# Performance work log

Hardware: AMD Instinct MI355X
Metric: run time of the kernel (lower is better)

## Reference

```python
import jax, jax.numpy as jnp
import numpy as np

B, C, N, M = 4096, 1024, 256, 64
EPS = 1e-8


def _linear_params(key, out_dim, in_dim):
    kw, kb = jax.random.split(key)
    lim = 1.0 / np.sqrt(in_dim)
    W = jax.random.uniform(kw, (out_dim, in_dim), jnp.float32, -lim, lim)
    b = jax.random.uniform(kb, (out_dim,), jnp.float32, -lim, lim)
    return W, b


def setup_inputs() -> dict:
    key = jax.random.key(0)
    ks = jax.random.split(key, 10)
    emb = jax.random.normal(ks[0], (B, C), jnp.float32)
    w_prev = jax.random.uniform(ks[1], (B, N), jnp.float32)
    w_prev = w_prev / jnp.sum(w_prev, axis=1, keepdims=True)  # valid weighting
    memory = jax.random.normal(ks[2], (B, N, M), jnp.float32) * 0.1
    Wk, bk = _linear_params(ks[3], M, C)
    Wbeta, bbeta = _linear_params(ks[4], 1, C)
    Wg, bg = _linear_params(ks[5], 1, C)
    Ws, bs = _linear_params(ks[6], 3, C)
    Wgamma, bgamma = _linear_params(ks[7], 1, C)
    We, be = _linear_params(ks[8], M, C)
    Wa, ba = _linear_params(ks[9], M, C)
    return {
        'embeddings': emb, 'w_prev': w_prev, 'memory': memory,
        'Wk': Wk, 'bk': bk, 'Wbeta': Wbeta, 'bbeta': bbeta,
        'Wg': Wg, 'bg': bg, 'Ws': Ws, 'bs': bs,
        'Wgamma': Wgamma, 'bgamma': bgamma,
        'We': We, 'be': be, 'Wa': Wa, 'ba': ba,
    }


def _forward(embeddings, w_prev, memory, Wk, bk, Wbeta, bbeta, Wg, bg,
             Ws, bs, Wgamma, bgamma, We, be, Wa, ba):
    k = embeddings @ Wk.T + bk                                  # [B, M]
    beta = jax.nn.softplus(embeddings @ Wbeta.T + bbeta)        # [B, 1]
    g = jax.nn.sigmoid(embeddings @ Wg.T + bg)                  # [B, 1]
    s = jax.nn.softmax(embeddings @ Ws.T + bs, axis=1)          # [B, 3]
    gamma = 1.0 + jax.nn.softplus(embeddings @ Wgamma.T + bgamma)  # [B, 1]
    e = jax.nn.sigmoid(embeddings @ We.T + be)                  # [B, M]
    a = embeddings @ Wa.T + ba                                  # [B, M]

    # content addressing: beta-scaled cosine similarity + softmax
    dot = jnp.einsum('bnm,bm->bn', memory, k)                   # [B, N]
    mem_norm = jnp.linalg.norm(memory, axis=-1)                 # [B, N]
    k_norm = jnp.linalg.norm(k, axis=-1, keepdims=True)         # [B, 1]
    cos = dot / (jnp.maximum(mem_norm, EPS) * jnp.maximum(k_norm, EPS))
    w_c = jax.nn.softmax(beta * cos, axis=1)                    # [B, N]

    # interpolation gate
    w_g = g * w_c + (1.0 - g) * w_prev                          # [B, N]

    # circular 3-tap shift: c[i] = s0*w[i-1] + s1*w[i] + s2*w[i+1]
    w_s = (s[:, 0:1] * jnp.roll(w_g, 1, axis=1)
           + s[:, 1:2] * w_g
           + s[:, 2:3] * jnp.roll(w_g, -1, axis=1))             # [B, N]

    # sharpen
    w_pow = jnp.power(w_s, gamma)                               # [B, N]
    w = w_pow / (jnp.sum(w_pow, axis=1, keepdims=True) + 1e-16)

    # erase / add write (outer products)
    erase = w[:, :, None] * e[:, None, :]                       # [B, N, M]
    add = w[:, :, None] * a[:, None, :]                         # [B, N, M]
    new_memory = memory * (1.0 - erase) + add
    return w, new_memory


def reference(embeddings, w_prev, memory, Wk, bk, Wbeta, bbeta, Wg, bg,
              Ws, bs, Wgamma, bgamma, We, be, Wa, ba):
    return _forward(embeddings, w_prev, memory, Wk, bk, Wbeta, bbeta,
                    Wg, bg, Ws, bs, Wgamma, bgamma, We, be, Wa, ba)
```

## Files before the change

### kernel.cpp

```cpp
#include <hip/hip_runtime.h>
#include <hip/hip_bf16.h>

#define B_DIM 4096
#define C_DIM 1024
#define N_DIM 256
#define M_DIM 64
#define GPAD  208
#define NG    198
#define EPSC  1e-8f
#define PDS   17

typedef __attribute__((ext_vector_type(8))) short bfrag_t;
typedef __attribute__((ext_vector_type(4))) float ffrag_t;

__device__ __forceinline__ short f2b(float f) {
    __hip_bfloat16 h = __float2bfloat16(f);
    return *reinterpret_cast<short*>(&h);
}
__device__ __forceinline__ float softplus_f(float x) {
    return fmaxf(x, 0.f) + log1pf(expf(-fabsf(x)));
}
__device__ __forceinline__ float sigmoid_f(float x) {
    return 1.f / (1.f + expf(-x));
}
__device__ __forceinline__ float warp_red_max(float v) {
#pragma unroll
    for (int off = 32; off; off >>= 1) v = fmaxf(v, __shfl_xor(v, off));
    return v;
}
__device__ __forceinline__ float warp_red_sum(float v) {
#pragma unroll
    for (int off = 32; off; off >>= 1) v += __shfl_xor(v, off);
    return v;
}

__global__ __launch_bounds__(256) void build_wcat(
    const float* __restrict__ Wk, const float* __restrict__ Wbeta,
    const float* __restrict__ Wg, const float* __restrict__ Ws,
    const float* __restrict__ Wgamma, const float* __restrict__ We,
    const float* __restrict__ Wa, short* __restrict__ wcat)
{
    int idx = blockIdx.x * 256 + threadIdx.x;
    if (idx >= GPAD * C_DIM) return;
    int n = idx >> 10, k = idx & (C_DIM - 1);
    float v;
    if (n < 64)        v = Wk[n * C_DIM + k];
    else if (n == 64)  v = Wbeta[k];
    else if (n == 65)  v = Wg[k];
    else if (n < 69)   v = Ws[(n - 66) * C_DIM + k];
    else if (n == 69)  v = Wgamma[k];
    else if (n < 134)  v = We[(n - 70) * C_DIM + k];
    else if (n < NG)   v = Wa[(n - 134) * C_DIM + k];
    else               v = 0.f;
    wcat[idx] = f2b(v);
}

__global__ __launch_bounds__(256) void cvt_emb(
    const float* __restrict__ emb, short* __restrict__ embh)
{
    int idx = (blockIdx.x * 256 + threadIdx.x) << 3;
    if (idx >= B_DIM * C_DIM) return;
    float4 a0 = *(const float4*)(emb + idx);
    float4 a1 = *(const float4*)(emb + idx + 4);
    bfrag_t f;
    f[0] = f2b(a0.x); f[1] = f2b(a0.y); f[2] = f2b(a0.z); f[3] = f2b(a0.w);
    f[4] = f2b(a1.x); f[5] = f2b(a1.y); f[6] = f2b(a1.z); f[7] = f2b(a1.w);
    *(bfrag_t*)(embh + idx) = f;
}

__global__ __launch_bounds__(256) void gates_gemm(
    const short* __restrict__ embh,
    const short* __restrict__ wcat,
    float* __restrict__ gates)
{
    const int wave = threadIdx.x >> 6;
    const int lane = threadIdx.x & 63;
    const int rg   = blockIdx.x >> 2;
    const int tt   = ((blockIdx.x & 3) << 2) + wave;
    if (tt >= 13) return;

    const int m  = lane & 15;
    const int ko = (lane >> 4) << 3;

    const short* arow = embh + (size_t)(rg * 16 + m) * C_DIM + ko;
    const short* brow = wcat + (size_t)(tt * 16 + m) * C_DIM + ko;

    ffrag_t acc = (ffrag_t)(0.f);
#pragma unroll 4
    for (int k = 0; k < C_DIM; k += 32) {
        bfrag_t af = *(const bfrag_t*)(arow + k);
        bfrag_t bf = *(const bfrag_t*)(brow + k);
        acc = __builtin_amdgcn_mfma_f32_16x16x32_bf16(af, bf, acc, 0, 0, 0);
    }

    const int crow = rg * 16 + ((lane >> 4) << 2);
    const int n = (tt << 4) + m;
#pragma unroll
    for (int rr = 0; rr < 4; ++rr)
        gates[(size_t)(crow + rr) * GPAD + n] = acc[rr];
}

__global__ __launch_bounds__(256, 4) void ntm_fused(
    const float* __restrict__ w_prev,
    const float* __restrict__ memory,
    const float* __restrict__ gates,
    const float* __restrict__ bk, const float* __restrict__ bbeta,
    const float* __restrict__ bg, const float* __restrict__ bs,
    const float* __restrict__ bgamma, const float* __restrict__ be,
    const float* __restrict__ ba,
    float* __restrict__ out_w,
    float* __restrict__ out_mem)
{
    const int b = blockIdx.x;
    const int t = threadIdx.x;
    const int r = t >> 4;
    const int c = t & 15;

    __shared__ __align__(16) float pdot[N_DIM * PDS];
    __shared__ __align__(16) float pnrm[N_DIM * PDS];
    __shared__ __align__(16) float pre[NG];
    __shared__ __align__(16) float kvf[M_DIM];
    __shared__ __align__(16) float ev[M_DIM];
    __shared__ __align__(16) float av[M_DIM];
    __shared__ float wgs[N_DIM];
    __shared__ float wsh[N_DIM];
    __shared__ float scal[8];
    __shared__ float redA[4], redB[4], redC[4];

    const float4* msrc = (const float4*)(memory + (size_t)b * (N_DIM * M_DIM));
    float4 v[16];
#pragma unroll
    for (int i = 0; i < 16; ++i) v[i] = msrc[t + (i << 8)];

    float wprev_t = w_prev[(size_t)b * N_DIM + t];
    if (t < NG) pre[t] = gates[(size_t)b * GPAD + t];
    __syncthreads();

    if (t < 64) {
        float kt = pre[t] + bk[t];
        kvf[t] = kt;
        ev[t]  = sigmoid_f(pre[70 + t] + be[t]);
        av[t]  = pre[134 + t] + ba[t];
        float sq = warp_red_sum(kt * kt);
        if (t == 0) scal[6] = sqrtf(sq);
    }
    if (t == 64) {
        scal[0] = softplus_f(pre[64] + bbeta[0]);
        scal[1] = sigmoid_f(pre[65] + bg[0]);
        float x0 = pre[66] + bs[0];
        float x1 = pre[67] + bs[1];
        float x2 = pre[68] + bs[2];
        float mxs = fmaxf(x0, fmaxf(x1, x2));
        float e0 = expf(x0 - mxs), e1 = expf(x1 - mxs), e2 = expf(x2 - mxs);
        float inv = 1.f / (e0 + e1 + e2);
        scal[3] = e0 * inv; scal[4] = e1 * inv; scal[5] = e2 * inv;
        scal[2] = 1.f + softplus_f(pre[69] + bgamma[0]);
    }
    __syncthreads();

    float4 kc = *(const float4*)&kvf[c << 2];
#pragma unroll
    for (int i = 0; i < 16; ++i) {
        float d, q;
        d = v[i].x * kc.x;          q = v[i].x * v[i].x;
        d = fmaf(v[i].y, kc.y, d);  q = fmaf(v[i].y, v[i].y, q);
        d = fmaf(v[i].z, kc.z, d);  q = fmaf(v[i].z, v[i].z, q);
        d = fmaf(v[i].w, kc.w, d);  q = fmaf(v[i].w, v[i].w, q);
        int n = r + (i << 4);
        pdot[n * PDS + c] = d;
        pnrm[n * PDS + c] = q;
    }
    __syncthreads();

    float dot = 0.f, nrm = 0.f;
#pragma unroll
    for (int j = 0; j < 16; ++j) {
        dot += pdot[t * PDS + j];
        nrm += pnrm[t * PDS + j];
    }

    float cosv = dot / (fmaxf(sqrtf(nrm), EPSC) * fmaxf(scal[6], EPSC));
    float x = scal[0] * cosv;

    float mx = warp_red_max(x);
    if ((t & 63) == 0) redA[t >> 6] = mx;
    __syncthreads();
    mx = fmaxf(fmaxf(redA[0], redA[1]), fmaxf(redA[2], redA[3]));
    float ex = expf(x - mx);
    float sm_ = warp_red_sum(ex);
    if ((t & 63) == 0) redB[t >> 6] = sm_;
    __syncthreads();
    float wc = ex / (redB[0] + redB[1] + redB[2] + redB[3]);

    float g = scal[1];
    float wg = g * wc + (1.f - g) * wprev_t;
    wgs[t] = wg;
    __syncthreads();

    float ws_ = scal[3] * wgs[(t + 255) & 255] + scal[4] * wg + scal[5] * wgs[(t + 1) & 255];

    float wp = powf(fmaxf(ws_, 0.f), scal[2]);
    float ts = warp_red_sum(wp);
    if ((t & 63) == 0) redC[t >> 6] = ts;
    __syncthreads();
    float w = wp / (redC[0] + redC[1] + redC[2] + redC[3] + 1e-16f);

    out_w[(size_t)b * N_DIM + t] = w;
    wsh[t] = w;
    __syncthreads();

    float4* omem = (float4*)(out_mem + (size_t)b * (N_DIM * M_DIM));
    float4 e4 = *(const float4*)&ev[c << 2];
    float4 a4 = *(const float4*)&av[c << 2];
#pragma unroll
    for (int i = 0; i < 16; ++i) {
        float wn = wsh[r + (i << 4)];
        float4 m_ = v[i];
        float4 rr;
        rr.x = fmaf(m_.x, -wn * e4.x, fmaf(wn, a4.x, m_.x));
        rr.y = fmaf(m_.y, -wn * e4.y, fmaf(wn, a4.y, m_.y));
        rr.z = fmaf(m_.z, -wn * e4.z, fmaf(wn, a4.z, m_.z));
        rr.w = fmaf(m_.w, -wn * e4.w, fmaf(wn, a4.w, m_.w));
        omem[t + (i << 8)] = rr;
    }
}

extern "C" void kernel_launch(void* const* d_in, const int* in_sizes, int n_in,
                              void* d_out, int out_size, void* d_ws, size_t ws_size,
                              hipStream_t stream) {
    const float* emb    = (const float*)d_in[0];
    const float* w_prev = (const float*)d_in[1];
    const float* memory = (const float*)d_in[2];
    const float* Wk     = (const float*)d_in[3];
    const float* bk     = (const float*)d_in[4];
    const float* Wbeta  = (const float*)d_in[5];
    const float* bbeta  = (const float*)d_in[6];
    const float* Wg     = (const float*)d_in[7];
    const float* bg     = (const float*)d_in[8];
    const float* Ws     = (const float*)d_in[9];
    const float* bs     = (const float*)d_in[10];
    const float* Wgamma = (const float*)d_in[11];
    const float* bgamma = (const float*)d_in[12];
    const float* We     = (const float*)d_in[13];
    const float* be     = (const float*)d_in[14];
    const float* Wa     = (const float*)d_in[15];
    const float* ba     = (const float*)d_in[16];

    const size_t WCAT_BYTES = (size_t)GPAD * C_DIM * sizeof(short);
    const size_t EMBH_BYTES = (size_t)B_DIM * C_DIM * sizeof(short);
    short* wcat  = (short*)d_ws;
    short* embh  = (short*)((char*)d_ws + WCAT_BYTES);
    float* gates = (float*)((char*)d_ws + WCAT_BYTES + EMBH_BYTES);

    float* out_w   = (float*)d_out;
    float* out_mem = out_w + (size_t)B_DIM * N_DIM;

    build_wcat<<<(GPAD * C_DIM + 255) / 256, 256, 0, stream>>>(
        Wk, Wbeta, Wg, Ws, Wgamma, We, Wa, wcat);
    cvt_emb<<<(B_DIM * C_DIM / 8 + 255) / 256, 256, 0, stream>>>(emb, embh);
    gates_gemm<<<(B_DIM / 16) * 4, 256, 0, stream>>>(embh, wcat, gates);
    ntm_fused<<<B_DIM, 256, 0, stream>>>(w_prev, memory, gates,
                                         bk, bbeta, bg, bs, bgamma, be, ba,
                                         out_w, out_mem);
}
```

Before: 521.1 us.

## Merge prep kernels, shuffle-reduce row dots, add nontemporal memory traffic

Merges the weight-packing and embedding-conversion kernels into one launch. In the fused kernel, the per-row dot and norm partials are now reduced with 16-lane shuffles instead of a large padded shared-memory scratch. This cuts LDS use and may raise occupancy. The memory tensor is read and written with nontemporal loads and stores, and the gates GEMM unroll goes from 4 to 8. Together these aim to reduce launch overhead, LDS traffic and cache pollution on the bandwidth-bound memory update, at the cost of more shuffle instructions.

```diff
diff --git a/kernel.cpp b/kernel.cpp
--- a/kernel.cpp
+++ b/kernel.cpp
@@ -8,10 +8,10 @@
 #define GPAD  208
 #define NG    198
 #define EPSC  1e-8f
-#define PDS   17
 
 typedef __attribute__((ext_vector_type(8))) short bfrag_t;
 typedef __attribute__((ext_vector_type(4))) float ffrag_t;
+typedef __attribute__((ext_vector_type(4))) float f4;
 
 __device__ __forceinline__ short f2b(float f) {
     __hip_bfloat16 h = __float2bfloat16(f);
@@ -33,39 +33,46 @@
     for (int off = 32; off; off >>= 1) v += __shfl_xor(v, off);
     return v;
 }
-
-__global__ __launch_bounds__(256) void build_wcat(
+__device__ __forceinline__ float red16_sum(float v) {
+#pragma unroll
+    for (int off = 8; off; off >>= 1) v += __shfl_xor(v, off);
+    return v;
+}
+
+#define PREP_A (GPAD * C_DIM)
+#define PREP_B (B_DIM * C_DIM / 8)
+__global__ __launch_bounds__(256) void prep(
     const float* __restrict__ Wk, const float* __restrict__ Wbeta,
     const float* __restrict__ Wg, const float* __restrict__ Ws,
     const float* __restrict__ Wgamma, const float* __restrict__ We,
-    const float* __restrict__ Wa, short* __restrict__ wcat)
+    const float* __restrict__ Wa, const float* __restrict__ emb,
+    short* __restrict__ wcat, short* __restrict__ embh)
 {
     int idx = blockIdx.x * 256 + threadIdx.x;
-    if (idx >= GPAD * C_DIM) return;
-    int n = idx >> 10, k = idx & (C_DIM - 1);
-    float v;
-    if (n < 64)        v = Wk[n * C_DIM + k];
-    else if (n == 64)  v = Wbeta[k];
-    else if (n == 65)  v = Wg[k];
-    else if (n < 69)   v = Ws[(n - 66) * C_DIM + k];
-    else if (n == 69)  v = Wgamma[k];
-    else if (n < 134)  v = We[(n - 70) * C_DIM + k];
-    else if (n < NG)   v = Wa[(n - 134) * C_DIM + k];
-    else               v = 0.f;
-    wcat[idx] = f2b(v);
-}
-
-__global__ __launch_bounds__(256) void cvt_emb(
-    const float* __restrict__ emb, short* __restrict__ embh)
-{
-    int idx = (blockIdx.x * 256 + threadIdx.x) << 3;
-    if (idx >= B_DIM * C_DIM) return;
-    float4 a0 = *(const float4*)(emb + idx);
-    float4 a1 = *(const float4*)(emb + idx + 4);
-    bfrag_t f;
-    f[0] = f2b(a0.x); f[1] = f2b(a0.y); f[2] = f2b(a0.z); f[3] = f2b(a0.w);
-    f[4] = f2b(a1.x); f[5] = f2b(a1.y); f[6] = f2b(a1.z); f[7] = f2b(a1.w);
-    *(bfrag_t*)(embh + idx) = f;
+    if (idx < PREP_A) {
+        int n = idx >> 10, k = idx & (C_DIM - 1);
+        float v;
+        if (n < 64)        v = Wk[n * C_DIM + k];
+        else if (n == 64)  v = Wbeta[k];
+        else if (n == 65)  v = Wg[k];
+        else if (n < 69)   v = Ws[(n - 66) * C_DIM + k];
+        else if (n == 69)  v = Wgamma[k];
+        else if (n < 134)  v = We[(n - 70) * C_DIM + k];
+        else if (n < NG)   v = Wa[(n - 134) * C_DIM + k];
+        else               v = 0.f;
+        wcat[idx] = f2b(v);
+        return;
+    }
+    int j = idx - PREP_A;
+    if (j < PREP_B) {
+        int base = j << 3;
+        f4 a0 = __builtin_nontemporal_load((const f4*)(emb + base));
+        f4 a1 = __builtin_nontemporal_load((const f4*)(emb + base + 4));
+        bfrag_t f;
+        f[0] = f2b(a0.x); f[1] = f2b(a0.y); f[2] = f2b(a0.z); f[3] = f2b(a0.w);
+        f[4] = f2b(a1.x); f[5] = f2b(a1.y); f[6] = f2b(a1.z); f[7] = f2b(a1.w);
+        *(bfrag_t*)(embh + base) = f;
+    }
 }
 
 __global__ __launch_bounds__(256) void gates_gemm(
@@ -86,7 +93,7 @@
     const short* brow = wcat + (size_t)(tt * 16 + m) * C_DIM + ko;
 
     ffrag_t acc = (ffrag_t)(0.f);
-#pragma unroll 4
+#pragma unroll 8
     for (int k = 0; k < C_DIM; k += 32) {
         bfrag_t af = *(const bfrag_t*)(arow + k);
         bfrag_t bf = *(const bfrag_t*)(brow + k);
@@ -116,21 +123,21 @@
     const int r = t >> 4;
     const int c = t & 15;
 
-    __shared__ __align__(16) float pdot[N_DIM * PDS];
-    __shared__ __align__(16) float pnrm[N_DIM * PDS];
     __shared__ __align__(16) float pre[NG];
     __shared__ __align__(16) float kvf[M_DIM];
     __shared__ __align__(16) float ev[M_DIM];
     __shared__ __align__(16) float av[M_DIM];
+    __shared__ __align__(16) float rowdot[272];
+    __shared__ __align__(16) float rownrm[272];
     __shared__ float wgs[N_DIM];
     __shared__ float wsh[N_DIM];
     __shared__ float scal[8];
     __shared__ float redA[4], redB[4], redC[4];
 
-    const float4* msrc = (const float4*)(memory + (size_t)b * (N_DIM * M_DIM));
-    float4 v[16];
-#pragma unroll
-    for (int i = 0; i < 16; ++i) v[i] = msrc[t + (i << 8)];
+    const f4* msrc = (const f4*)(memory + (size_t)b * (N_DIM * M_DIM));
+    f4 v[16];
+#pragma unroll
+    for (int i = 0; i < 16; ++i) v[i] = __builtin_nontemporal_load(msrc + t + (i << 8));
 
     float wprev_t = w_prev[(size_t)b * N_DIM + t];
     if (t < NG) pre[t] = gates[(size_t)b * GPAD + t];
@@ -158,70 +165,73 @@
     }
     __syncthreads();
 
-    float4 kc = *(const float4*)&kvf[c << 2];
+    f4 kc = ((const f4*)kvf)[c];
+    float dkeep = 0.f, nkeep = 0.f;
 #pragma unroll
     for (int i = 0; i < 16; ++i) {
-        float d, q;
-        d = v[i].x * kc.x;          q = v[i].x * v[i].x;
-        d = fmaf(v[i].y, kc.y, d);  q = fmaf(v[i].y, v[i].y, q);
-        d = fmaf(v[i].z, kc.z, d);  q = fmaf(v[i].z, v[i].z, q);
-        d = fmaf(v[i].w, kc.w, d);  q = fmaf(v[i].w, v[i].w, q);
-        int n = r + (i << 4);
-        pdot[n * PDS + c] = d;
-        pnrm[n * PDS + c] = q;
-    }
-    __syncthreads();
-
-    float dot = 0.f, nrm = 0.f;
-#pragma unroll
-    for (int j = 0; j < 16; ++j) {
-        dot += pdot[t * PDS + j];
-        nrm += pnrm[t * PDS + j];
-    }
-
-    float cosv = dot / (fmaxf(sqrtf(nrm), EPSC) * fmaxf(scal[6], EPSC));
-    float x = scal[0] * cosv;
-
-    float mx = warp_red_max(x);
-    if ((t & 63) == 0) redA[t >> 6] = mx;
-    __syncthreads();
-    mx = fmaxf(fmaxf(redA[0], redA[1]), fmaxf(redA[2], redA[3]));
-    float ex = expf(x - mx);
-    float sm_ = warp_red_sum(ex);
-    if ((t & 63) == 0) redB[t >> 6] = sm_;
-    __syncthreads();
-    float wc = ex / (redB[0] + redB[1] + redB[2] + redB[3]);
-
-    float g = scal[1];
-    float wg = g * wc + (1.f - g) * wprev_t;
-    wgs[t] = wg;
-    __syncthreads();
-
-    float ws_ = scal[3] * wgs[(t + 255) & 255] + scal[4] * wg + scal[5] * wgs[(t + 1) & 255];
-
-    float wp = powf(fmaxf(ws_, 0.f), scal[2]);
-    float ts = warp_red_sum(wp);
-    if ((t & 63) == 0) redC[t >> 6] = ts;
-    __syncthreads();
-    float w = wp / (redC[0] + redC[1] + redC[2] + redC[3] + 1e-16f);
-
-    out_w[(size_t)b * N_DIM + t] = w;
-    wsh[t] = w;
-    __syncthreads();
-
-    float4* omem = (float4*)(out_mem + (size_t)b * (N_DIM * M_DIM));
-    float4 e4 = *(const float4*)&ev[c << 2];
-    float4 a4 = *(const float4*)&av[c << 2];
+        float d = v[i].x * kc.x,          q = v[i].x * v[i].x;
+        d = fmaf(v[i].y, kc.y, d);        q = fmaf(v[i].y, v[i].y, q);
+        d = fmaf(v[i].z, kc.z, d);        q = fmaf(v[i].z, v[i].z, q);
+        d = fmaf(v[i].w, kc.w, d);        q = fmaf(v[i].w, v[i].w, q);
+        d = red16_sum(d);                 q = red16_sum(q);
+        if (c == i) { dkeep = d; nkeep = q; }
+    }
+    {
+        int nsel = r + (c << 4);
+        int fi = nsel + (nsel >> 4);
+        rowdot[fi] = dkeep;
+        rownrm[fi] = nkeep;
+    }
+    __syncthreads();
+
+    {
+        int ft = t + (t >> 4);
+        float dot = rowdot[ft], nrm = rownrm[ft];
+        float cosv = dot / (fmaxf(sqrtf(nrm), EPSC) * fmaxf(scal[6], EPSC));
+        float x = scal[0] * cosv;
+
+        float mx = warp_red_max(x);
+        if ((t & 63) == 0) redA[t >> 6] = mx;
+        __syncthreads();
+        mx = fmaxf(fmaxf(redA[0], redA[1]), fmaxf(redA[2], redA[3]));
+        float ex = expf(x - mx);
+        float sm_ = warp_red_sum(ex);
+        if ((t & 63) == 0) redB[t >> 6] = sm_;
+        __syncthreads();
+        float wc = ex / (redB[0] + redB[1] + redB[2] + redB[3]);
+
+        float g = scal[1];
+        float wg = g * wc + (1.f - g) * wprev_t;
+        wgs[t] = wg;
+        __syncthreads();
+
+        float ws_ = scal[3] * wgs[(t + 255) & 255] + scal[4] * wg
+                  + scal[5] * wgs[(t + 1) & 255];
+
+        float wp = powf(fmaxf(ws_, 0.f), scal[2]);
+        float ts = warp_red_sum(wp);
+        if ((t & 63) == 0) redC[t >> 6] = ts;
+        __syncthreads();
+        float w = wp / (redC[0] + redC[1] + redC[2] + redC[3] + 1e-16f);
+
+        out_w[(size_t)b * N_DIM + t] = w;
+        wsh[t] = w;
+    }
+    __syncthreads();
+
+    f4* omem = (f4*)(out_mem + (size_t)b * (N_DIM * M_DIM));
+    f4 e4 = ((const f4*)ev)[c];
+    f4 a4 = ((const f4*)av)[c];
 #pragma unroll
     for (int i = 0; i < 16; ++i) {
         float wn = wsh[r + (i << 4)];
-        float4 m_ = v[i];
-        float4 rr;
+        f4 m_ = v[i];
+        f4 rr;
         rr.x = fmaf(m_.x, -wn * e4.x, fmaf(wn, a4.x, m_.x));
         rr.y = fmaf(m_.y, -wn * e4.y, fmaf(wn, a4.y, m_.y));
         rr.z = fmaf(m_.z, -wn * e4.z, fmaf(wn, a4.z, m_.z));
         rr.w = fmaf(m_.w, -wn * e4.w, fmaf(wn, a4.w, m_.w));
-        omem[t + (i << 8)] = rr;
+        __builtin_nontemporal_store(rr, omem + t + (i << 8));
     }
 }
 
@@ -255,9 +265,8 @@
     float* out_w   = (float*)d_out;
     float* out_mem = out_w + (size_t)B_DIM * N_DIM;
 
-    build_wcat<<<(GPAD * C_DIM + 255) / 256, 256, 0, stream>>>(
-        Wk, Wbeta, Wg, Ws, Wgamma, We, Wa, wcat);
-    cvt_emb<<<(B_DIM * C_DIM / 8 + 255) / 256, 256, 0, stream>>>(emb, embh);
+    prep<<<(PREP_A + PREP_B + 255) / 256, 256, 0, stream>>>(
+        Wk, Wbeta, Wg, Ws, Wgamma, We, Wa, emb, wcat, embh);
     gates_gemm<<<(B_DIM / 16) * 4, 256, 0, stream>>>(embh, wcat, gates);
     ntm_fused<<<B_DIM, 256, 0, stream>>>(w_prev, memory, gates,
                                          bk, bbeta, bg, bs, bgamma, be, ba,
```

Result: faster. 506.8 us (-2.8%).
